# Kernel optimization log

Hardware: AMD Instinct MI355X
Metric: run time of the kernel (lower is better)

Reference implementation:

```python
import jax, jax.numpy as jnp
import numpy as np

N_Q = 4; K = 4; IMG = 28; PAD = IMG + 2  # pad right/bottom so edge windows exist
N_WIN = 14 * 14  # stride-2 windows over 28x28


def _window_idx():
    # Faithful to torch: flatten the (possibly truncated) window row-major,
    # then pad with zeros AT THE END of the flattened vector.
    zero = PAD * PAD - 1  # padded image is zero there
    rows = []
    for i in range(0, IMG - 1, 2):
        for j in range(0, IMG - 1, 2):
            h = min(K, IMG - i); w = min(K, IMG - j)
            ids = [(i + r) * PAD + (j + c) for r in range(h) for c in range(w)]
            ids += [zero] * (K * K - len(ids))
            rows.append(ids)
    return np.asarray(rows, np.int32)  # [196, 16]

_WIDX = _window_idx()
# wire 0 is the most-significant bit of the 16-dim statevector index
_BITS = ((np.arange(16)[None, :] >> (3 - np.arange(4))[:, None]) & 1)
_ZSIGN = (1.0 - 2.0 * _BITS).astype(np.float32)  # [4, 16] PauliZ eigenvalues
# Four CRZ gates (control i, target (i+1)%4) are all diagonal -> combined diagonal phase
_CRZ_SIGNS = np.zeros(16, np.float32)
for _b in range(16):
    s = 0
    for _i in range(4):
        c = (_b >> (3 - _i)) & 1
        t = (_b >> (3 - ((_i + 1) % 4))) & 1
        s += c * (2 * t - 1)
    _CRZ_SIGNS[_b] = s
_H = (np.array([[1, 1], [1, -1]], np.complex64) / np.sqrt(2.0)).astype(np.complex64)


def _rz(a):  # a [B] -> [B,2,2]: diag(e^{-i a/2}, e^{+i a/2})
    em = jnp.exp(-0.5j * a); ep = jnp.exp(0.5j * a); z = jnp.zeros_like(em)
    return jnp.stack([jnp.stack([em, z], -1), jnp.stack([z, ep], -1)], -2)


def _ry(a):  # a [...] -> [...,2,2]
    c = jnp.cos(0.5 * a); s = jnp.sin(0.5 * a)
    return jnp.stack([jnp.stack([c, -s], -1), jnp.stack([s, c], -1)], -2).astype(jnp.complex64)


def _apply1q(state, U, w):  # state [B,16], U [B,2,2] or [2,2], wire w (0=MSB)
    L = 2 ** w; R = 2 ** (3 - w)
    s = state.reshape(-1, L, 2, R)
    if U.ndim == 2:
        out = jnp.einsum('ij,bajc->baic', U, s)
    else:
        out = jnp.einsum('bij,bajc->baic', U, s)
    return out.reshape(-1, 16)


def reference(x, crz_theta, ry_theta, fc1_w, fc1_b, fc2_w, fc2_b):
    B = x.shape[0]
    xp = jnp.pad(x[:, 0], ((0, 0), (0, 2), (0, 2))).reshape(B, -1)  # [B, 900]
    wins = xp[:, jnp.asarray(_WIDX)]              # [B, 196, 16]
    wins = jnp.transpose(wins, (1, 0, 2))         # [196, B, 16] for scan

    crz_diag = jnp.exp(0.5j * crz_theta * jnp.asarray(_CRZ_SIGNS))  # [16]
    Ry = _ry(ry_theta)                            # shared trainable RY, [2,2]
    H = jnp.asarray(_H)
    zsT = jnp.asarray(_ZSIGN).T                   # [16, 4]

    def step(state, f):  # state [B,16] complex64 persists ACROSS windows (no reset in source)
        for w in range(4):
            # compose H then the encoder rotations on this wire into one 2x2 per batch elem
            U = jnp.broadcast_to(H, (B, 2, 2))
            n = 5 if w < 3 else 1  # wire 3 only gets rz(f[15])
            for i in range(n):
                a = f[:, w * 5 + i]
                M = _rz(a) if i % 2 == 0 else _ry(a)  # gates = rz,ry,rz,ry,rz
                U = jnp.einsum('bij,bjk->bik', M, U)
            state = _apply1q(state, U, w)
        state = state * crz_diag[None, :]          # ring of CRZ gates (diagonal)
        for w in range(4):
            state = _apply1q(state, Ry, w)
        probs = state.real ** 2 + state.imag ** 2
        return state, probs @ zsT                  # [B, 4] PauliZ expectations

    state0 = jnp.zeros((B, 16), jnp.complex64).at[:, 0].set(1.0)
    _, outs = jax.lax.scan(step, state0, wins)     # [196, B, 4]
    feats = jnp.transpose(outs, (1, 0, 2)).reshape(B, N_WIN * 4)  # window-major concat
    h1 = feats @ fc1_w.T + fc1_b
    h1 = jnp.where(h1 > 0, h1, 0.1 * h1)           # LeakyReLU(0.1)
    return h1 @ fc2_w.T + fc2_b


def setup_inputs() -> dict:
    key = jax.random.key(0)
    ks = jax.random.split(key, 7)
    B = 16384
    return {
        'x': jax.random.normal(ks[0], (B, 1, 28, 28), jnp.float32),
        'crz_theta': jax.random.normal(ks[1], (), jnp.float32),
        'ry_theta': jax.random.normal(ks[2], (), jnp.float32),
        'fc1_w': jax.random.normal(ks[3], (20, 784), jnp.float32) * 0.03,
        'fc1_b': jnp.zeros((20,), jnp.float32),
        'fc2_w': jax.random.normal(ks[4], (2, 20), jnp.float32) * 0.1,
        'fc2_b': jnp.zeros((2,), jnp.float32),
    }
```

## Files before the change

### kernel.cpp

```cpp
#include <hip/hip_runtime.h>

#define RS2f 0.70710678118654752f

#define QP_XOR1 0xB1
#define QP_XOR2 0x4E
#define QP_BC0  0x00
#define QP_BC1  0x55
#define QP_BC2  0xAA
#define QP_BC3  0xFF

template<int CTRL> __device__ __forceinline__ float dppf(float x) {
  return __int_as_float(__builtin_amdgcn_update_dpp(
      0, __float_as_int(x), CTRL, 0xF, 0xF, true));
}

__device__ __forceinline__ float sxor(float x, int sm) {
  return __int_as_float(__float_as_int(x) ^ sm);
}

__device__ __forceinline__ void build_gate(float a0, float a1, float a2, float a3, float a4,
                                           float &w0r, float &w0i, float &w1r, float &w1i) {
  float s, c;
  __sincosf(0.5f*a0, &s, &c);
  float ar = c, ai = -s, br = 0.f, bi = 0.f;
  __sincosf(0.5f*a1, &s, &c);
  { float tar = c*ar + s*br, tai = c*ai - s*bi;
    float tbr = c*br - s*ar, tbi = c*bi + s*ai;
    ar=tar; ai=tai; br=tbr; bi=tbi; }
  __sincosf(0.5f*a2, &s, &c);
  { float t;
    t=ar; ar = c*t + s*ai; ai = c*ai - s*t;
    t=br; br = c*t + s*bi; bi = c*bi - s*t; }
  __sincosf(0.5f*a3, &s, &c);
  { float tar = c*ar + s*br, tai = c*ai - s*bi;
    float tbr = c*br - s*ar, tbi = c*bi + s*ai;
    ar=tar; ai=tai; br=tbr; bi=tbi; }
  __sincosf(0.5f*a4, &s, &c);
  { float t;
    t=ar; ar = c*t + s*ai; ai = c*ai - s*t;
    t=br; br = c*t + s*bi; bi = c*bi - s*t; }
  w0r = RS2f*(ar+br); w0i = RS2f*(ai+bi);
  w1r = RS2f*(ar-br); w1i = RS2f*(ai-bi);
}

#define PICK_FULL                                                            \
  a0 = l0 ? P[0][0] : l1 ? P[1][1] : l2 ? P[2][2] : P[3][3];                 \
  a1 = l0 ? P[0][1] : l1 ? P[1][2] : l2 ? P[2][3] : 0.f;                     \
  a2 = l0 ? P[0][2] : l1 ? P[1][3] : l2 ? P[3][0] : 0.f;                     \
  a3 = l0 ? P[0][3] : l1 ? P[2][0] : l2 ? P[3][1] : 0.f;                     \
  a4 = l0 ? P[1][0] : l1 ? P[2][1] : l2 ? P[3][2] : 0.f;

#define PICK_W2                                                              \
  a0 = l0 ? P[0][0] : l1 ? P[2][1] : 0.f;                                    \
  a1 = l0 ? P[0][1] : l1 ? P[3][0] : 0.f;                                    \
  a2 = l0 ? P[1][0] : l1 ? P[3][1] : 0.f;                                    \
  a3 = l0 ? P[1][1] : 0.f;                                                   \
  a4 = l0 ? P[2][0] : 0.f;

#define PICK_H2                                                              \
  a0 = l0 ? P[0][0] : l1 ? P[1][1] : 0.f;                                    \
  a1 = l0 ? P[0][1] : l1 ? P[1][2] : 0.f;                                    \
  a2 = l0 ? P[0][2] : l1 ? P[1][3] : 0.f;                                    \
  a3 = l0 ? P[0][3] : 0.f;                                                   \
  a4 = l0 ? P[1][0] : 0.f;

#define PICK_22                                                              \
  a0 = l0 ? P[0][0] : 0.f;                                                   \
  a1 = l0 ? P[0][1] : 0.f;                                                   \
  a2 = l0 ? P[1][0] : 0.f;                                                   \
  a3 = l0 ? P[1][1] : 0.f;                                                   \
  a4 = 0.f;

#define APPLY_AND_FOLD(WIN) do {                                             \
  { float w0r = dppf<QP_BC0>(Wc0), w0i = dppf<QP_BC0>(Wc1);                  \
    float w1r = dppf<QP_BC0>(Wc2), w1i = dppf<QP_BC0>(Wc3);                  \
    float uar = sxor(w0r, sm0), uai = w0i;                                   \
    float ubr = w1r,            ubi = sxor(w1i, sm0);                        \
    _Pragma("unroll")                                                        \
    for (int k = 0; k < 4; ++k) {                                            \
      float pr = dppf<QP_XOR2>(sr[k]), pi = dppf<QP_XOR2>(si[k]);            \
      float ar = sr[k], ai = si[k];                                          \
      sr[k] = uar*ar - uai*ai + ubr*pr - ubi*pi;                             \
      si[k] = uar*ai + uai*ar + ubr*pi + ubi*pr;                             \
    } }                                                                      \
  { float w0r = dppf<QP_BC1>(Wc0), w0i = dppf<QP_BC1>(Wc1);                  \
    float w1r = dppf<QP_BC1>(Wc2), w1i = dppf<QP_BC1>(Wc3);                  \
    float uar = sxor(w0r, sm1), uai = w0i;                                   \
    float ubr = w1r,            ubi = sxor(w1i, sm1);                        \
    _Pragma("unroll")                                                        \
    for (int k = 0; k < 4; ++k) {                                            \
      float pr = dppf<QP_XOR1>(sr[k]), pi = dppf<QP_XOR1>(si[k]);            \
      float ar = sr[k], ai = si[k];                                          \
      sr[k] = uar*ar - uai*ai + ubr*pr - ubi*pi;                             \
      si[k] = uar*ai + uai*ar + ubr*pi + ubi*pr;                             \
    } }                                                                      \
  { float w0r = dppf<QP_BC2>(Wc0), w0i = dppf<QP_BC2>(Wc1);                  \
    float w1r = dppf<QP_BC2>(Wc2), w1i = dppf<QP_BC2>(Wc3);                  \
    _Pragma("unroll")                                                        \
    for (int k = 0; k < 2; ++k) {                                            \
      float lr = sr[k], li = si[k], hr = sr[k+2], hi = si[k+2];              \
      sr[k]   = w0r*lr - w0i*li + w1r*hr - w1i*hi;                           \
      si[k]   = w0r*li + w0i*lr + w1r*hi + w1i*hr;                           \
      sr[k+2] = w1r*lr + w1i*li - w0r*hr - w0i*hi;                           \
      si[k+2] = w1r*li - w1i*lr - w0r*hi + w0i*hr;                           \
    } }                                                                      \
  { float w0r = dppf<QP_BC3>(Wc0), w0i = dppf<QP_BC3>(Wc1);                  \
    float w1r = dppf<QP_BC3>(Wc2), w1i = dppf<QP_BC3>(Wc3);                  \
    _Pragma("unroll")                                                        \
    for (int k = 0; k < 4; k += 2) {                                         \
      float lr = sr[k], li = si[k], hr = sr[k+1], hi = si[k+1];              \
      sr[k]   = w0r*lr - w0i*li + w1r*hr - w1i*hi;                           \
      si[k]   = w0r*li + w0i*lr + w1r*hi + w1i*hr;                           \
      sr[k+1] = w1r*lr + w1i*li - w0r*hr - w0i*hi;                           \
      si[k+1] = w1r*li - w1i*lr - w0r*hi + w0i*hr;                           \
    } }                                                                      \
  _Pragma("unroll")                                                          \
  for (int k = 0; k < 4; ++k) {                                              \
    float r_ = sr[k], im_ = si[k];                                           \
    sr[k] = czk[k]*r_ - szk[k]*im_;                                          \
    si[k] = czk[k]*im_ + szk[k]*r_;                                          \
  }                                                                          \
  _Pragma("unroll")                                                          \
  for (int k = 0; k < 4; ++k) {                                              \
    float pr = dppf<QP_XOR2>(sr[k]), pi = dppf<QP_XOR2>(si[k]);              \
    sr[k] = cry*sr[k] + sgn0*pr;                                             \
    si[k] = cry*si[k] + sgn0*pi;                                             \
  }                                                                          \
  _Pragma("unroll")                                                          \
  for (int k = 0; k < 4; ++k) {                                              \
    float pr = dppf<QP_XOR1>(sr[k]), pi = dppf<QP_XOR1>(si[k]);              \
    sr[k] = cry*sr[k] + sgn1*pr;                                             \
    si[k] = cry*si[k] + sgn1*pi;                                             \
  }                                                                          \
  _Pragma("unroll")                                                          \
  for (int k = 0; k < 2; ++k) {                                              \
    float ar=sr[k], br2=sr[k+2]; sr[k]=cry*ar - sry*br2; sr[k+2]=sry*ar + cry*br2; \
    float ai=si[k], bi2=si[k+2]; si[k]=cry*ai - sry*bi2; si[k+2]=sry*ai + cry*bi2; \
  }                                                                          \
  _Pragma("unroll")                                                          \
  for (int k = 0; k < 4; k += 2) {                                           \
    float ar=sr[k], br2=sr[k+1]; sr[k]=cry*ar - sry*br2; sr[k+1]=sry*ar + cry*br2; \
    float ai=si[k], bi2=si[k+1]; si[k]=cry*ai - sry*bi2; si[k+1]=sry*ai + cry*bi2; \
  }                                                                          \
  { float p0 = sr[0]*sr[0] + si[0]*si[0];                                    \
    float p1 = sr[1]*sr[1] + si[1]*si[1];                                    \
    float p2 = sr[2]*sr[2] + si[2]*si[2];                                    \
    float p3 = sr[3]*sr[3] + si[3]*si[3];                                    \
    float s01 = p0 + p1, s23 = p2 + p3;                                      \
    float t_  = s01 + s23;                                                   \
    float o0 = sxor(t_, sm0);                                                \
    float o1 = sxor(t_, sm1);                                                \
    float o2 = s01 - s23;                                                    \
    float o3 = (p0 - p1) + (p2 - p3);                                        \
    o0 += dppf<QP_XOR1>(o0); o0 += dppf<QP_XOR2>(o0);                        \
    o1 += dppf<QP_XOR1>(o1); o1 += dppf<QP_XOR2>(o1);                        \
    o2 += dppf<QP_XOR1>(o2); o2 += dppf<QP_XOR2>(o2);                        \
    o3 += dppf<QP_XOR1>(o3); o3 += dppf<QP_XOR2>(o3);                        \
    const int win4_ = (WIN) * 4;                                             \
    _Pragma("unroll")                                                        \
    for (int j = 0; j < 5; ++j) {                                            \
      float4 wv = *(const float4*)(swl + j * 784 + win4_);                   \
      h1[j] = fmaf(wv.x, o0, fmaf(wv.y, o1, fmaf(wv.z, o2, fmaf(wv.w, o3, h1[j])))); \
    } }                                                                      \
} while (0)

#define ROTATE_W  Wc0 = Wn0; Wc1 = Wn1; Wc2 = Wn2; Wc3 = Wn3;

__global__ void __launch_bounds__(256)
quanv_kernel(const float* __restrict__ x,
             const float* __restrict__ crz_t,
             const float* __restrict__ ry_t,
             const float* __restrict__ fc1_w,
             const float* __restrict__ fc1_b,
             const float* __restrict__ fc2_w,
             const float* __restrict__ fc2_b,
             float* __restrict__ out, int B)
{
  __shared__ float sw[20 * 784];
  const int tid = threadIdx.x;
  for (int i = tid; i < (20 * 784) / 4; i += 256)
    ((float4*)sw)[i] = ((const float4*)fc1_w)[i];
  __syncthreads();

  const int l = tid & 3;
  const int b = (blockIdx.x * 256 + tid) >> 2;
  if (b >= B) return;
  const float* img = x + (size_t)b * 784;
  const bool l0 = (l == 0), l1 = (l == 1), l2 = (l == 2);

  const float theta = crz_t[0];
  const float ryt   = ry_t[0];
  float cry, sry;
  __sincosf(0.5f * ryt, &sry, &cry);
  const float sgn0 = (l & 2) ? sry : -sry;
  const float sgn1 = (l & 1) ? sry : -sry;
  const int sm0 = (l & 2) ? (int)0x80000000 : 0;
  const int sm1 = (l & 1) ? (int)0x80000000 : 0;

  float g0,g1,g2,g3;
  if      (l == 0) { g0= 0.f; g1=-1.f; g2=-1.f; g3=0.f; }
  else if (l == 1) { g0=-1.f; g1=-2.f; g2= 0.f; g3=1.f; }
  else if (l == 2) { g0=-1.f; g1= 0.f; g2=-2.f; g3=1.f; }
  else             { g0= 0.f; g1= 1.f; g2= 1.f; g3=4.f; }
  float czk[4], szk[4];
  __sincosf(0.5f*theta*g0, &szk[0], &czk[0]);
  __sincosf(0.5f*theta*g1, &szk[1], &czk[1]);
  __sincosf(0.5f*theta*g2, &szk[2], &czk[2]);
  __sincosf(0.5f*theta*g3, &szk[3], &czk[3]);

  float sr[4], si[4];
#pragma unroll
  for (int k = 0; k < 4; ++k) { sr[k] = 0.f; si[k] = 0.f; }
  if (l == 0) sr[0] = 1.f;

  float h1[5];
#pragma unroll
  for (int j = 0; j < 5; ++j) h1[j] = 0.f;
  const float* swl = sw + 5 * l * 784;

  float P[4][4];
  float a0, a1, a2, a3, a4;
  float Wc0, Wc1, Wc2, Wc3, Wn0, Wn1, Wn2, Wn3;

#pragma unroll 1
  for (int wi = 0; wi < 13; ++wi) {
    const float* imgw = img + (2 * wi) * 28;

#pragma unroll
    for (int r = 0; r < 4; ++r) {
      float4 v = *(const float4*)(imgw + r * 28);
      P[r][0]=v.x; P[r][1]=v.y; P[r][2]=v.z; P[r][3]=v.w;
    }
    PICK_FULL;
    build_gate(a0, a1, a2, a3, a4, Wc0, Wc1, Wc2, Wc3);

#pragma unroll 1
    for (int wj = 1; wj <= 12; ++wj) {
      const int c0 = 2 * wj + 2;
#pragma unroll
      for (int r = 0; r < 4; ++r) {
        P[r][0] = P[r][2]; P[r][1] = P[r][3];
        float2 v = *(const float2*)(imgw + r * 28 + c0);
        P[r][2] = v.x; P[r][3] = v.y;
      }
      PICK_FULL;
      build_gate(a0, a1, a2, a3, a4, Wn0, Wn1, Wn2, Wn3);
      APPLY_AND_FOLD(wi * 14 + wj - 1);
      ROTATE_W;
    }

#pragma unroll
    for (int r = 0; r < 4; ++r) {
      P[r][0] = P[r][2]; P[r][1] = P[r][3]; P[r][2] = 0.f; P[r][3] = 0.f;
    }
    PICK_W2;
    build_gate(a0, a1, a2, a3, a4, Wn0, Wn1, Wn2, Wn3);
    APPLY_AND_FOLD(wi * 14 + 12);
    ROTATE_W;
    APPLY_AND_FOLD(wi * 14 + 13);
  }

  {
    const float* imgw = img + 26 * 28;
#pragma unroll
    for (int r = 0; r < 2; ++r) {
      float4 v = *(const float4*)(imgw + r * 28);
      P[r][0]=v.x; P[r][1]=v.y; P[r][2]=v.z; P[r][3]=v.w;
    }
#pragma unroll
    for (int r = 2; r < 4; ++r) { P[r][0]=0.f; P[r][1]=0.f; P[r][2]=0.f; P[r][3]=0.f; }
    PICK_H2;
    build_gate(a0, a1, a2, a3, a4, Wc0, Wc1, Wc2, Wc3);

#pragma unroll 1
    for (int wj = 1; wj <= 12; ++wj) {
      const int c0 = 2 * wj + 2;
      P[0][0]=P[0][2]; P[0][1]=P[0][3];
      P[1][0]=P[1][2]; P[1][1]=P[1][3];
      float2 v0 = *(const float2*)(imgw + c0);       P[0][2]=v0.x; P[0][3]=v0.y;
      float2 v1 = *(const float2*)(imgw + 28 + c0);  P[1][2]=v1.x; P[1][3]=v1.y;
      PICK_H2;
      build_gate(a0, a1, a2, a3, a4, Wn0, Wn1, Wn2, Wn3);
      APPLY_AND_FOLD(182 + wj - 1);
      ROTATE_W;
    }

    P[0][0]=P[0][2]; P[0][1]=P[0][3]; P[0][2]=0.f; P[0][3]=0.f;
    P[1][0]=P[1][2]; P[1][1]=P[1][3]; P[1][2]=0.f; P[1][3]=0.f;
    PICK_22;
    build_gate(a0, a1, a2, a3, a4, Wn0, Wn1, Wn2, Wn3);
    APPLY_AND_FOLD(182 + 12);
    ROTATE_W;
    APPLY_AND_FOLD(182 + 13);
  }

  float pa = 0.f, pb = 0.f;
#pragma unroll
  for (int j = 0; j < 5; ++j) {
    const int r = 5 * l + j;
    float v = h1[j] + fc1_b[r];
    v = (v > 0.f) ? v : 0.1f * v;
    pa = fmaf(fc2_w[r],      v, pa);
    pb = fmaf(fc2_w[20 + r], v, pb);
  }
  pa += dppf<QP_XOR1>(pa); pa += dppf<QP_XOR2>(pa);
  pb += dppf<QP_XOR1>(pb); pb += dppf<QP_XOR2>(pb);
  if (l == 0) {
    float2 res; res.x = pa + fc2_b[0]; res.y = pb + fc2_b[1];
    *(float2*)(out + (size_t)b * 2) = res;
  }
}

extern "C" void kernel_launch(void* const* d_in, const int* in_sizes, int n_in,
                              void* d_out, int out_size, void* d_ws, size_t ws_size,
                              hipStream_t stream) {
  const float* x      = (const float*)d_in[0];
  const float* crz_t  = (const float*)d_in[1];
  const float* ry_t   = (const float*)d_in[2];
  const float* fc1_w  = (const float*)d_in[3];
  const float* fc1_b  = (const float*)d_in[4];
  const float* fc2_w  = (const float*)d_in[5];
  const float* fc2_b  = (const float*)d_in[6];
  float* out = (float*)d_out;
  const int B = in_sizes[0] / 784;
  const int grid = (B * 4 + 255) / 256;
  quanv_kernel<<<grid, 256, 0, stream>>>(x, crz_t, ry_t, fc1_w, fc1_b,
                                         fc2_w, fc2_b, out, B);
}
```

Measured before the change: 252.4 us.

## Pack complex amplitudes into float2 for packed FMA and simplify gate construction

Stores each complex amplitude as a two-wide float vector so the gate applications can lower to packed FMA instructions (v_pk_fma_f32) on CDNA. It also rewrites the per-window gate builder so that the RZ/RY/RZ/RY/RZ product plus Hadamard comes from closed-form sums and differences of angles. This replaces the sequential rotation composition with five sincos calls and a few FMAs. The swizzles (vperp) and the per-component DPP calls may add extra moves that offset the packed-math gain, and the new gate algebra must match the old one exactly.

```diff
diff --git a/kernel.cpp b/kernel.cpp
--- a/kernel.cpp
+++ b/kernel.cpp
@@ -9,38 +9,43 @@
 #define QP_BC2  0xAA
 #define QP_BC3  0xFF
 
+typedef float v2f __attribute__((ext_vector_type(2)));
+
 template<int CTRL> __device__ __forceinline__ float dppf(float x) {
   return __int_as_float(__builtin_amdgcn_update_dpp(
       0, __float_as_int(x), CTRL, 0xF, 0xF, true));
 }
+template<int CTRL> __device__ __forceinline__ v2f dpp2(v2f v) {
+  v2f r; r.x = dppf<CTRL>(v.x); r.y = dppf<CTRL>(v.y); return r;
+}
 
 __device__ __forceinline__ float sxor(float x, int sm) {
   return __int_as_float(__float_as_int(x) ^ sm);
 }
+__device__ __forceinline__ v2f vsplat(float a) { v2f r; r.x = a; r.y = a; return r; }
+__device__ __forceinline__ v2f vperp(v2f v) { v2f r; r.x = -v.y; r.y = v.x; return r; }
+__device__ __forceinline__ v2f vperc(v2f v) { v2f r; r.x = v.y; r.y = -v.x; return r; }
+__device__ __forceinline__ v2f vfma2(float a, v2f b, v2f c) {
+  return __builtin_elementwise_fma(vsplat(a), b, c);
+}
+__device__ __forceinline__ v2f vmul2(float a, v2f b) { return vsplat(a) * b; }
 
 __device__ __forceinline__ void build_gate(float a0, float a1, float a2, float a3, float a4,
                                            float &w0r, float &w0i, float &w1r, float &w1i) {
-  float s, c;
-  __sincosf(0.5f*a0, &s, &c);
-  float ar = c, ai = -s, br = 0.f, bi = 0.f;
-  __sincosf(0.5f*a1, &s, &c);
-  { float tar = c*ar + s*br, tai = c*ai - s*bi;
-    float tbr = c*br - s*ar, tbi = c*bi + s*ai;
-    ar=tar; ai=tai; br=tbr; bi=tbi; }
-  __sincosf(0.5f*a2, &s, &c);
-  { float t;
-    t=ar; ar = c*t + s*ai; ai = c*ai - s*t;
-    t=br; br = c*t + s*bi; bi = c*bi - s*t; }
-  __sincosf(0.5f*a3, &s, &c);
-  { float tar = c*ar + s*br, tai = c*ai - s*bi;
-    float tbr = c*br - s*ar, tbi = c*bi + s*ai;
-    ar=tar; ai=tai; br=tbr; bi=tbi; }
-  __sincosf(0.5f*a4, &s, &c);
-  { float t;
-    t=ar; ar = c*t + s*ai; ai = c*ai - s*t;
-    t=br; br = c*t + s*bi; bi = c*bi - s*t; }
-  w0r = RS2f*(ar+br); w0i = RS2f*(ai+bi);
-  w1r = RS2f*(ar-br); w1i = RS2f*(ai-bi);
+  float sBp, cBp, sBm, cBm, sC, cC, sP, cP, sM, cM;
+  __sincosf(0.5f * (a1 + a3), &sBp, &cBp);
+  __sincosf(0.5f * (a1 - a3), &sBm, &cBm);
+  __sincosf(0.5f * a2,        &sC,  &cC);
+  __sincosf(0.5f * (a0 + a4), &sP,  &cP);
+  __sincosf(0.5f * (a0 - a4), &sM,  &cM);
+  float m00r =  cBp * cC, m00i = -cBm * sC;
+  float m01r = -sBp * cC, m01i =  sBm * sC;
+  float alr = fmaf(m00r, cP,  m00i * sP);
+  float ali = fmaf(m00i, cP, -m00r * sP);
+  float ber = fmaf(m01r, cM, -m01i * sM);
+  float bei = fmaf(m01i, cM,  m01r * sM);
+  w0r = RS2f * (alr + ber); w0i = RS2f * (ali + bei);
+  w1r = RS2f * (alr - ber); w1i = RS2f * (ali - bei);
 }
 
 #define PICK_FULL                                                            \
@@ -72,80 +77,86 @@
   a4 = 0.f;
 
 #define APPLY_AND_FOLD(WIN) do {                                             \
+                                \
   { float w0r = dppf<QP_BC0>(Wc0), w0i = dppf<QP_BC0>(Wc1);                  \
     float w1r = dppf<QP_BC0>(Wc2), w1i = dppf<QP_BC0>(Wc3);                  \
     float uar = sxor(w0r, sm0), uai = w0i;                                   \
     float ubr = w1r,            ubi = sxor(w1i, sm0);                        \
     _Pragma("unroll")                                                        \
     for (int k = 0; k < 4; ++k) {                                            \
-      float pr = dppf<QP_XOR2>(sr[k]), pi = dppf<QP_XOR2>(si[k]);            \
-      float ar = sr[k], ai = si[k];                                          \
-      sr[k] = uar*ar - uai*ai + ubr*pr - ubi*pi;                             \
-      si[k] = uar*ai + uai*ar + ubr*pi + ubi*pr;                             \
-    } }                                                                      \
+      v2f p = dpp2<QP_XOR2>(s[k]);                                           \
+      v2f a = s[k];                                                          \
+      s[k] = vfma2(uar, a, vfma2(uai, vperp(a),                              \
+                   vfma2(ubr, p, vmul2(ubi, vperp(p)))));                    \
+    } }                                                                      \
+                                 \
   { float w0r = dppf<QP_BC1>(Wc0), w0i = dppf<QP_BC1>(Wc1);                  \
     float w1r = dppf<QP_BC1>(Wc2), w1i = dppf<QP_BC1>(Wc3);                  \
     float uar = sxor(w0r, sm1), uai = w0i;                                   \
     float ubr = w1r,            ubi = sxor(w1i, sm1);                        \
     _Pragma("unroll")                                                        \
     for (int k = 0; k < 4; ++k) {                                            \
-      float pr = dppf<QP_XOR1>(sr[k]), pi = dppf<QP_XOR1>(si[k]);            \
-      float ar = sr[k], ai = si[k];                                          \
-      sr[k] = uar*ar - uai*ai + ubr*pr - ubi*pi;                             \
-      si[k] = uar*ai + uai*ar + ubr*pi + ubi*pr;                             \
-    } }                                                                      \
+      v2f p = dpp2<QP_XOR1>(s[k]);                                           \
+      v2f a = s[k];                                                          \
+      s[k] = vfma2(uar, a, vfma2(uai, vperp(a),                              \
+                   vfma2(ubr, p, vmul2(ubi, vperp(p)))));                    \
+    } }                                                                      \
+   \
   { float w0r = dppf<QP_BC2>(Wc0), w0i = dppf<QP_BC2>(Wc1);                  \
     float w1r = dppf<QP_BC2>(Wc2), w1i = dppf<QP_BC2>(Wc3);                  \
+    float nw0r = -w0r, nw0i = -w0i;                                          \
     _Pragma("unroll")                                                        \
     for (int k = 0; k < 2; ++k) {                                            \
-      float lr = sr[k], li = si[k], hr = sr[k+2], hi = si[k+2];              \
-      sr[k]   = w0r*lr - w0i*li + w1r*hr - w1i*hi;                           \
-      si[k]   = w0r*li + w0i*lr + w1r*hi + w1i*hr;                           \
-      sr[k+2] = w1r*lr + w1i*li - w0r*hr - w0i*hi;                           \
-      si[k+2] = w1r*li - w1i*lr - w0r*hi + w0i*hr;                           \
-    } }                                                                      \
+      v2f lo = s[k], hi = s[k+2];                                            \
+      s[k]   = vfma2(w0r, lo, vfma2(w0i, vperp(lo),                          \
+                     vfma2(w1r, hi, vmul2(w1i, vperp(hi)))));                \
+      s[k+2] = vfma2(w1r, lo, vfma2(w1i, vperc(lo),                          \
+                     vfma2(nw0r, hi, vmul2(nw0i, vperc(hi)))));              \
+    } }                                                                      \
+                                           \
   { float w0r = dppf<QP_BC3>(Wc0), w0i = dppf<QP_BC3>(Wc1);                  \
     float w1r = dppf<QP_BC3>(Wc2), w1i = dppf<QP_BC3>(Wc3);                  \
+    float nw0r = -w0r, nw0i = -w0i;                                          \
     _Pragma("unroll")                                                        \
     for (int k = 0; k < 4; k += 2) {                                         \
-      float lr = sr[k], li = si[k], hr = sr[k+1], hi = si[k+1];              \
-      sr[k]   = w0r*lr - w0i*li + w1r*hr - w1i*hi;                           \
-      si[k]   = w0r*li + w0i*lr + w1r*hi + w1i*hr;                           \
-      sr[k+1] = w1r*lr + w1i*li - w0r*hr - w0i*hi;                           \
-      si[k+1] = w1r*li - w1i*lr - w0r*hi + w0i*hr;                           \
-    } }                                                                      \
+      v2f lo = s[k], hi = s[k+1];                                            \
+      s[k]   = vfma2(w0r, lo, vfma2(w0i, vperp(lo),                          \
+                     vfma2(w1r, hi, vmul2(w1i, vperp(hi)))));                \
+      s[k+1] = vfma2(w1r, lo, vfma2(w1i, vperc(lo),                          \
+                     vfma2(nw0r, hi, vmul2(nw0i, vperc(hi)))));              \
+    } }                                                                      \
+                                    \
+  _Pragma("unroll")                                                          \
+  for (int k = 0; k < 4; ++k)                                                \
+    s[k] = vfma2(czk[k], s[k], vmul2(szk[k], vperp(s[k])));                  \
+                                              \
   _Pragma("unroll")                                                          \
   for (int k = 0; k < 4; ++k) {                                              \
-    float r_ = sr[k], im_ = si[k];                                           \
-    sr[k] = czk[k]*r_ - szk[k]*im_;                                          \
-    si[k] = czk[k]*im_ + szk[k]*r_;                                          \
+    v2f p = dpp2<QP_XOR2>(s[k]);                                             \
+    s[k] = vfma2(cry, s[k], vmul2(sgn0, p));                                 \
   }                                                                          \
   _Pragma("unroll")                                                          \
   for (int k = 0; k < 4; ++k) {                                              \
-    float pr = dppf<QP_XOR2>(sr[k]), pi = dppf<QP_XOR2>(si[k]);              \
-    sr[k] = cry*sr[k] + sgn0*pr;                                             \
-    si[k] = cry*si[k] + sgn0*pi;                                             \
+    v2f p = dpp2<QP_XOR1>(s[k]);                                             \
+    s[k] = vfma2(cry, s[k], vmul2(sgn1, p));                                 \
   }                                                                          \
-  _Pragma("unroll")                                                          \
-  for (int k = 0; k < 4; ++k) {                                              \
-    float pr = dppf<QP_XOR1>(sr[k]), pi = dppf<QP_XOR1>(si[k]);              \
-    sr[k] = cry*sr[k] + sgn1*pr;                                             \
-    si[k] = cry*si[k] + sgn1*pi;                                             \
+                                                   \
+  _Pragma("unroll")                                                          \
+  for (int k = 0; k < 2; ++k) {                                              \
+    v2f lo = s[k], hi = s[k+2];                                              \
+    s[k]   = vfma2(cry, lo, vmul2(nsry, hi));                                \
+    s[k+2] = vfma2(sry, lo, vmul2(cry, hi));                                 \
   }                                                                          \
   _Pragma("unroll")                                                          \
-  for (int k = 0; k < 2; ++k) {                                              \
-    float ar=sr[k], br2=sr[k+2]; sr[k]=cry*ar - sry*br2; sr[k+2]=sry*ar + cry*br2; \
-    float ai=si[k], bi2=si[k+2]; si[k]=cry*ai - sry*bi2; si[k+2]=sry*ai + cry*bi2; \
+  for (int k = 0; k < 4; k += 2) {                                           \
+    v2f lo = s[k], hi = s[k+1];                                              \
+    s[k]   = vfma2(cry, lo, vmul2(nsry, hi));                                \
+    s[k+1] = vfma2(sry, lo, vmul2(cry, hi));                                 \
   }                                                                          \
-  _Pragma("unroll")                                                          \
-  for (int k = 0; k < 4; k += 2) {                                           \
-    float ar=sr[k], br2=sr[k+1]; sr[k]=cry*ar - sry*br2; sr[k+1]=sry*ar + cry*br2; \
-    float ai=si[k], bi2=si[k+1]; si[k]=cry*ai - sry*bi2; si[k+1]=sry*ai + cry*bi2; \
-  }                                                                          \
-  { float p0 = sr[0]*sr[0] + si[0]*si[0];                                    \
-    float p1 = sr[1]*sr[1] + si[1]*si[1];                                    \
-    float p2 = sr[2]*sr[2] + si[2]*si[2];                                    \
-    float p3 = sr[3]*sr[3] + si[3]*si[3];                                    \
+                                        \
+  { v2f q0 = s[0]*s[0], q1 = s[1]*s[1], q2 = s[2]*s[2], q3 = s[3]*s[3];      \
+    float p0 = q0.x + q0.y, p1 = q1.x + q1.y;                                \
+    float p2 = q2.x + q2.y, p3 = q3.x + q3.y;                                \
     float s01 = p0 + p1, s23 = p2 + p3;                                      \
     float t_  = s01 + s23;                                                   \
     float o0 = sxor(t_, sm0);                                                \
@@ -192,6 +203,7 @@
   const float ryt   = ry_t[0];
   float cry, sry;
   __sincosf(0.5f * ryt, &sry, &cry);
+  const float nsry = -sry;
   const float sgn0 = (l & 2) ? sry : -sry;
   const float sgn1 = (l & 1) ? sry : -sry;
   const int sm0 = (l & 2) ? (int)0x80000000 : 0;
@@ -208,10 +220,10 @@
   __sincosf(0.5f*theta*g2, &szk[2], &czk[2]);
   __sincosf(0.5f*theta*g3, &szk[3], &czk[3]);
 
-  float sr[4], si[4];
-#pragma unroll
-  for (int k = 0; k < 4; ++k) { sr[k] = 0.f; si[k] = 0.f; }
-  if (l == 0) sr[0] = 1.f;
+  v2f s[4];
+#pragma unroll
+  for (int k = 0; k < 4; ++k) { s[k].x = 0.f; s[k].y = 0.f; }
+  if (l == 0) s[0].x = 1.f;
 
   float h1[5];
 #pragma unroll
```

After: 225.0 us. 10.8% less time.
